# Performance work log

Measured on AMD Instinct MI355X. Metric: run time of the kernel, lower is better.

Reference implementation:

```python
import jax, jax.numpy as jnp
import numpy as np

DIM = 256
HEADS = 8
DHEAD = 64
MEM = 4
HID = HEADS * DHEAD  # 512


def setup_inputs() -> dict:
    key = jax.random.key(0)
    k1, k2, k3, k4 = jax.random.split(key, 4)
    x = jax.random.normal(k1, (2, DIM, 48, 48), jnp.float32)
    gamma = jnp.zeros((DIM, 1, 1), jnp.float32)  # nn.Parameter init is zeros
    mem_kv = jax.random.normal(k2, (2, HEADS, MEM, DHEAD), jnp.float32)
    w_qkv = jax.random.normal(k3, (3 * HID, DIM), jnp.float32) * 0.05  # 1x1 conv weight
    w_out = jax.random.normal(k4, (DIM, HID), jnp.float32) * 0.05     # 1x1 conv weight
    return {"x": x, "gamma": gamma, "mem_kv": mem_kv, "w_qkv": w_qkv, "w_out": w_out}


def reference(x, gamma, mem_kv, w_qkv, w_out):
    b, c, h, w = x.shape
    scale = DHEAD ** -0.5
    # RMSNorm: F.normalize along channel dim (L2, eps=1e-12) * (gamma+1) * sqrt(dim)
    l2 = jnp.sqrt(jnp.sum(x * x, axis=1, keepdims=True))
    xn = x / jnp.maximum(l2, 1e-12) * (gamma + 1.0) * (c ** 0.5)
    # 1x1 conv to qkv: [b, 3*HID, h, w]
    qkv = jnp.einsum('oc,bchw->bohw', w_qkv, xn)
    qkv = qkv.reshape(b, 3, HEADS, DHEAD, h * w)
    # (b, heads, n, dhead)
    q = jnp.swapaxes(qkv[:, 0], 2, 3)
    k = jnp.swapaxes(qkv[:, 1], 2, 3)
    v = jnp.swapaxes(qkv[:, 2], 2, 3)
    # prepend learnable memory kv tokens
    mk = jnp.broadcast_to(mem_kv[0], (b, HEADS, MEM, DHEAD))
    mv = jnp.broadcast_to(mem_kv[1], (b, HEADS, MEM, DHEAD))
    k = jnp.concatenate([mk, k], axis=2)
    v = jnp.concatenate([mv, v], axis=2)
    sim = jnp.einsum('bhid,bhjd->bhij', q * scale, k)
    attn = jax.nn.softmax(sim, axis=-1)
    out = jnp.einsum('bhij,bhjd->bhid', attn, v)
    out = jnp.swapaxes(out, 2, 3).reshape(b, HID, h, w)
    return jnp.einsum('oc,bchw->bohw', w_out, out)
```

## Files before the change

### kernel.cpp

```cpp
#include <hip/hip_runtime.h>

#define BATCH 2
#define CDIM 256
#define NPIX 2304
#define NHEAD 8
#define DH 64
#define HID 512
#define NMEM 4
#define NKV 2308
#define NKVP 2368
#define QSCALE 0.125f
#define LOG2E 1.4426950408889634f
#define WQKV_E 393216
#define WOUT_E 131072
#define KVSPLIT 1216

typedef float f32x4 __attribute__((ext_vector_type(4)));
typedef __bf16 bf16x8 __attribute__((ext_vector_type(8)));
typedef unsigned short u16;
typedef u16 u16x4 __attribute__((ext_vector_type(4)));
typedef u16 u16x8 __attribute__((ext_vector_type(8)));
typedef unsigned u32x2 __attribute__((ext_vector_type(2)));

#if __has_builtin(__builtin_amdgcn_exp2f)
#define EXP2(x) __builtin_amdgcn_exp2f(x)
#else
#define EXP2(x) exp2f(x)
#endif

static __device__ __forceinline__ u16 f2b(float f) {
  union { float f; unsigned u; } a; a.f = f;
  unsigned u = a.u;
  u += 0x7fffu + ((u >> 16) & 1u);
  return (u16)(u >> 16);
}

__global__ __launch_bounds__(256) void k_prep(
    const float* __restrict__ wqkv, const float* __restrict__ wout,
    const float* __restrict__ gamma, const float* __restrict__ mem_kv,
    u16* __restrict__ wb, u16* __restrict__ kk, u16* __restrict__ vT)
{
  const int blk = blockIdx.x, t = threadIdx.x;
  if (blk < 256) {
    const int i0 = (blk * 256 + t) * 8;
    u16x8 o;
    if (i0 < WQKV_E) {
      const float sc = ((i0 >> 8) < 512) ? QSCALE * LOG2E : 1.0f;
      const int c0 = i0 & 255;
      const f32x4 a = *(const f32x4*)&wqkv[i0];
      const f32x4 b = *(const f32x4*)&wqkv[i0 + 4];
      const f32x4 g0 = *(const f32x4*)&gamma[c0];
      const f32x4 g1 = *(const f32x4*)&gamma[c0 + 4];
#pragma unroll
      for (int e = 0; e < 4; ++e) {
        o[e]     = f2b(a[e] * sc * (1.0f + g0[e]));
        o[e + 4] = f2b(b[e] * sc * (1.0f + g1[e]));
      }
    } else {
      const f32x4 a = *(const f32x4*)&wout[i0 - WQKV_E];
      const f32x4 b = *(const f32x4*)&wout[i0 - WQKV_E + 4];
#pragma unroll
      for (int e = 0; e < 4; ++e) { o[e] = f2b(a[e]); o[e + 4] = f2b(b[e]); }
    }
    *(u16x8*)&wb[i0] = o;
  } else if (blk < 272) {
    const int idx = (blk - 256) * 256 + t;
    const int d = idx & 63;
    const int m = (idx >> 6) & 3;
    const int h = (idx >> 8) & 7;
    const int b = idx >> 11;
    const float mk = mem_kv[((size_t)h * NMEM + m) * DH + d];
    const float mv = mem_kv[(((size_t)NHEAD + h) * NMEM + m) * DH + d];
    kk[(((size_t)(b * NHEAD + h)) * NKV + m) * DH + d] = f2b(mk);
    vT[(((size_t)(b * NHEAD + h)) * DH + d) * NKVP + m] = f2b(mv);
  } else {
    const int gid = (blk - 272) * 256 + t;
    const int row = gid >> 4;
    const int c0 = (gid & 15) * 4 + 2304;
    u16x4 z = {0, 0, 0, 0};
    *(u16x4*)&vT[(size_t)row * NKVP + c0] = z;
  }
}

__global__ __launch_bounds__(256) void k_norm(
    const float* __restrict__ x, u16* __restrict__ xnT)
{
  __shared__ float xs[16 * 261];
  __shared__ float red[16][17];
  __shared__ float rsh[16];
  const int t = threadIdx.x;
  const int blk = blockIdx.x;
  const int b = blk / 144;
  const int p0 = (blk % 144) * 16;
  const int px = t & 15, cg = t >> 4;
  const float* xb = x + (size_t)b * CDIM * NPIX + p0 + px;
  float ssq = 0.f;
#pragma unroll
  for (int i = 0; i < 16; ++i) {
    const int c = cg * 16 + i;
    const float v = xb[(size_t)c * NPIX];
    xs[px * 261 + c] = v;
    ssq += v * v;
  }
  red[px][cg] = ssq;
  __syncthreads();
  if (t < 16) {
    float s = 0.f;
#pragma unroll
    for (int i = 0; i < 16; ++i) s += red[t][i];
    rsh[t] = 16.0f / fmaxf(sqrtf(s), 1e-12f);
  }
  __syncthreads();
  {
    const int pp = t >> 4, c0 = (t & 15) * 16;
    const float rs = rsh[pp];
    u16x8 o0, o1;
#pragma unroll
    for (int e = 0; e < 8; ++e) {
      o0[e] = f2b(xs[pp * 261 + c0 + e] * rs);
      o1[e] = f2b(xs[pp * 261 + c0 + 8 + e] * rs);
    }
    u16* dst = &xnT[(size_t)(b * NPIX + p0 + pp) * CDIM + c0];
    *(u16x8*)dst = o0;
    *(u16x8*)(dst + 8) = o1;
  }
}

__global__ __launch_bounds__(256) void k_qkv(
    const u16* __restrict__ xnT, const u16* __restrict__ wb,
    u16* __restrict__ q, u16* __restrict__ kk, u16* __restrict__ vT)
{
  __shared__ __align__(16) u16 bs[64 * 256];
  const int t = threadIdx.x, w = t >> 6, l = t & 63, li = l & 15, kg = l >> 4;
  const int m0 = blockIdx.x * 64 + w * 16;
  const int n0 = blockIdx.y * 64;
  {
    const int brow = t >> 2, bcs = (t & 3) * 64;
    const int bsw = (brow & 7) * 8;
    const u16* wsrc = wb + (size_t)(n0 + brow) * CDIM + bcs;
#pragma unroll
    for (int j = 0; j < 8; ++j) {
      const u16x8 v = *(const u16x8*)&wsrc[j * 8];
      *(u16x8*)&bs[brow * 256 + ((bcs + j * 8) ^ bsw)] = v;
    }
  }
  const u16* ap = xnT + (size_t)(m0 + li) * CDIM + kg * 8;
  const int lsw = (li & 7) * 8;
  f32x4 acc[4];
#pragma unroll
  for (int cf = 0; cf < 4; ++cf) { f32x4 z = {0.f,0.f,0.f,0.f}; acc[cf] = z; }
  __syncthreads();
#pragma unroll
  for (int ks = 0; ks < 8; ++ks) {
    const bf16x8 af = *(const bf16x8*)(ap + ks * 32);
#pragma unroll
    for (int cf = 0; cf < 4; ++cf) {
      const int row = cf * 16 + li;
      const bf16x8 bfr = *(const bf16x8*)&bs[row * 256 + ((ks * 32 + kg * 8) ^ lsw)];
      acc[cf] = __builtin_amdgcn_mfma_f32_16x16x32_bf16(af, bfr, acc[cf], 0, 0, 0);
    }
  }
  const int bb = (m0 >= NPIX) ? 1 : 0;
  const int plbase = m0 - bb * NPIX + kg * 4;
#pragma unroll
  for (int cf = 0; cf < 4; ++cf) {
    const int o0f = n0 + cf * 16;
    const int r = o0f >> 9, oo = o0f & 511, h = oo >> 6, d = (oo & 63) + li;
    if (r == 0) {
      u16* base = q + ((size_t)(bb * NHEAD + h) * NPIX + plbase) * DH + d;
#pragma unroll
      for (int rr = 0; rr < 4; ++rr) base[(size_t)rr * DH] = f2b(acc[cf][rr]);
    } else if (r == 1) {
      u16* base = kk + ((size_t)(bb * NHEAD + h) * NKV + NMEM + plbase) * DH + d;
#pragma unroll
      for (int rr = 0; rr < 4; ++rr) base[(size_t)rr * DH] = f2b(acc[cf][rr]);
    } else {
      u16x4 pk;
#pragma unroll
      for (int rr = 0; rr < 4; ++rr) pk[rr] = f2b(acc[cf][rr]);
      *(u16x4*)&vT[(((size_t)(bb * NHEAD + h)) * DH + d) * NKVP + NMEM + plbase] = pk;
    }
  }
}

__global__ __launch_bounds__(512) void k_attn(
    const u16* __restrict__ q, const u16* __restrict__ kk, const u16* __restrict__ vT,
    u16* __restrict__ aoB)
{
  __shared__ __align__(16) char smem[51200];
  u16* kbuf = (u16*)smem;
  u16* vbuf = (u16*)(smem + 16384);
  u16* ps   = (u16*)(smem + 32768);
  float* accbuf = (float*)smem;
  float* mlbuf  = (float*)(smem + 17152);
  const int t = threadIdx.x;
  const int w = t >> 6, l = t & 63;
  const int qsub = w & 3, hf = w >> 2;
  const int li = l & 15, kg = l >> 4;
  const int id = blockIdx.x;
  const int xcd = id & 7, slot = id >> 3;
  const int yl = (slot >= 36) ? 1 : 0;
  const int xq = slot - yl * 36;
  const int bh = xcd * 2 + yl;
  const int b = bh >> 3, hh = bh & 7;
  const int qrow0 = xq * 64 + qsub * 16;
  const u16* qp = q + ((size_t)bh * NPIX + qrow0) * DH;
  const u16* kp = kk + (size_t)bh * NKV * DH;
  const u16* vp = vT + (size_t)bh * DH * NKVP;

  const bf16x8 bq0 = *(const bf16x8*)&qp[li * DH + kg * 8];
  const bf16x8 bq1 = *(const bf16x8*)&qp[li * DH + 32 + kg * 8];

  const int hft = t >> 8;
  const int tt = t & 255;
  const int srow = tt >> 3;
  const int scol = (tt & 7) * 8;
  const int ssw = (srow & 7) * 8;
  const int sbase = hft * KVSPLIT;
  u16* kdst0 = &kbuf[hft * 4096 + srow * 64 + (scol ^ ssw)];
  u16* kdst1 = &kbuf[hft * 4096 + (srow + 32) * 64 + (scol ^ ssw)];
  u16* vdst0 = &vbuf[hft * 4096 + srow * 64 + (scol ^ ssw)];
  u16* vdst1 = &vbuf[hft * 4096 + (srow + 32) * 64 + (scol ^ ssw)];

  f32x4 acc[4];
#pragma unroll
  for (int df = 0; df < 4; ++df) { f32x4 z = {0.f,0.f,0.f,0.f}; acc[df] = z; }
  float m = -1e30f, lsum = 0.f;
  const int cbase0 = hf * KVSPLIT;

  u16x8 rk0, rk1, rv0, rv1;
  rk0 = *(const u16x8*)&kp[(size_t)(sbase + srow) * DH + scol];
  rk1 = *(const u16x8*)&kp[(size_t)(sbase + srow + 32) * DH + scol];
  rv0 = *(const u16x8*)&vp[(size_t)srow * NKVP + sbase + scol];
  rv1 = *(const u16x8*)&vp[(size_t)(srow + 32) * NKVP + sbase + scol];

  const int NT = 19;
  for (int i = 0; i < NT; ++i) {
    __syncthreads();
    *(u16x8*)kdst0 = rk0;
    *(u16x8*)kdst1 = rk1;
    *(u16x8*)vdst0 = rv0;
    *(u16x8*)vdst1 = rv1;
    if (i + 1 < NT) {
      int nb = sbase + (i + 1) * 64;
      int snb = (nb > NKVP - 64) ? (NKVP - 64) : nb;
      int kr0 = nb + srow;      if (kr0 > NKV - 1) kr0 = NKV - 1;
      int kr1 = nb + srow + 32; if (kr1 > NKV - 1) kr1 = NKV - 1;
      rk0 = *(const u16x8*)&kp[(size_t)kr0 * DH + scol];
      rk1 = *(const u16x8*)&kp[(size_t)kr1 * DH + scol];
      rv0 = *(const u16x8*)&vp[(size_t)srow * NKVP + snb + scol];
      rv1 = *(const u16x8*)&vp[(size_t)(srow + 32) * NKVP + snb + scol];
    }
    __syncthreads();
    const int kbase = cbase0 + i * 64;
    if (kbase < NKV) {
      const bool lastt = (kbase + 64 > NKV);
      const u16* kb = &kbuf[hf * 4096];
      const u16* vb = &vbuf[hf * 4096];
      f32x4 s[4];
#pragma unroll
      for (int jf = 0; jf < 4; ++jf) {
        const int row = jf * 16 + li;
        const int rsw = (row & 7) * 8;
        const bf16x8 ak0 = *(const bf16x8*)&kb[row * 64 + ((kg * 8) ^ rsw)];
        const bf16x8 ak1 = *(const bf16x8*)&kb[row * 64 + ((32 + kg * 8) ^ rsw)];
        f32x4 sf = {0.f, 0.f, 0.f, 0.f};
        sf = __builtin_amdgcn_mfma_f32_16x16x32_bf16(ak0, bq0, sf, 0, 0, 0);
        sf = __builtin_amdgcn_mfma_f32_16x16x32_bf16(ak1, bq1, sf, 0, 0, 0);
        s[jf] = sf;
      }
      if (lastt) {
#pragma unroll
        for (int jf = 0; jf < 4; ++jf)
#pragma unroll
          for (int r = 0; r < 4; ++r)
            if (kbase + jf * 16 + kg * 4 + r >= NKV) s[jf][r] = -1e30f;
      }
      float pmax = fmaxf(fmaxf(fmaxf(s[0][0], s[0][1]), fmaxf(s[0][2], s[0][3])),
                         fmaxf(fmaxf(s[1][0], s[1][1]), fmaxf(s[1][2], s[1][3])));
      pmax = fmaxf(pmax, fmaxf(fmaxf(fmaxf(s[2][0], s[2][1]), fmaxf(s[2][2], s[2][3])),
                               fmaxf(fmaxf(s[3][0], s[3][1]), fmaxf(s[3][2], s[3][3]))));
      pmax = fmaxf(pmax, __shfl_xor(pmax, 16));
      pmax = fmaxf(pmax, __shfl_xor(pmax, 32));
      if (__any(pmax > m + 8.0f)) {
        const float mn = fmaxf(m, pmax);
        const float al = EXP2(m - mn);
        m = mn;
        lsum *= al;
        float a4[4];
#pragma unroll
        for (int r = 0; r < 4; ++r) a4[r] = __shfl(al, (l & 48) | (kg * 4 + r));
#pragma unroll
        for (int df = 0; df < 4; ++df)
#pragma unroll
          for (int r = 0; r < 4; ++r) acc[df][r] *= a4[r];
      }
#pragma unroll
      for (int jf = 0; jf < 4; ++jf) {
        u32x2 wp;
#pragma unroll
        for (int rp = 0; rp < 2; ++rp) {
          const float e0 = EXP2(s[jf][rp * 2 + 0] - m);
          const float e1 = EXP2(s[jf][rp * 2 + 1] - m);
          lsum += e0 + e1;
          unsigned pk;
          asm("v_cvt_pk_bf16_f32 %0, %1, %2" : "=v"(pk) : "v"(e0), "v"(e1));
          wp[rp] = pk;
        }
        *(u32x2*)&ps[w * 1152 + li * 72 + jf * 16 + kg * 4] = wp;
      }
      asm volatile("s_waitcnt lgkmcnt(0)" ::: "memory");
      __builtin_amdgcn_sched_barrier(0);
      const bf16x8 ap0 = *(const bf16x8*)&ps[w * 1152 + li * 72 + kg * 8];
      const bf16x8 ap1 = *(const bf16x8*)&ps[w * 1152 + li * 72 + 32 + kg * 8];
#pragma unroll
      for (int df = 0; df < 4; ++df) {
        const int row = df * 16 + li;
        const int rsw = (row & 7) * 8;
        const bf16x8 bv0 = *(const bf16x8*)&vb[row * 64 + ((kg * 8) ^ rsw)];
        const bf16x8 bv1 = *(const bf16x8*)&vb[row * 64 + ((32 + kg * 8) ^ rsw)];
        acc[df] = __builtin_amdgcn_mfma_f32_16x16x32_bf16(ap0, bv0, acc[df], 0, 0, 0);
        acc[df] = __builtin_amdgcn_mfma_f32_16x16x32_bf16(ap1, bv1, acc[df], 0, 0, 0);
      }
    }
  }
  lsum += __shfl_xor(lsum, 16);
  lsum += __shfl_xor(lsum, 32);
  float m4[4], l4[4];
#pragma unroll
  for (int r = 0; r < 4; ++r) {
    const int src = (l & 48) | (kg * 4 + r);
    m4[r] = __shfl(m, src);
    l4[r] = __shfl(lsum, src);
  }
  __syncthreads();
  if (hf == 1) {
#pragma unroll
    for (int df = 0; df < 4; ++df)
#pragma unroll
      for (int r = 0; r < 4; ++r)
        accbuf[(qsub * 16 + kg * 4 + r) * 67 + df * 16 + li] = acc[df][r];
    if (kg == 0) {
      mlbuf[(qsub * 16 + li) * 2 + 0] = m;
      mlbuf[(qsub * 16 + li) * 2 + 1] = lsum;
    }
  }
  __syncthreads();
  if (hf == 0) {
    float f0[4], f1[4], rL[4];
#pragma unroll
    for (int r = 0; r < 4; ++r) {
      const float m1 = mlbuf[(qsub * 16 + kg * 4 + r) * 2 + 0];
      const float l1 = mlbuf[(qsub * 16 + kg * 4 + r) * 2 + 1];
      const float M = fmaxf(m4[r], m1);
      f0[r] = EXP2(m4[r] - M);
      f1[r] = EXP2(m1 - M);
      rL[r] = __builtin_amdgcn_rcpf(l4[r] * f0[r] + l1 * f1[r]);
    }
#pragma unroll
    for (int df = 0; df < 4; ++df)
#pragma unroll
      for (int r = 0; r < 4; ++r) {
        const float a1 = accbuf[(qsub * 16 + kg * 4 + r) * 67 + df * 16 + li];
        const float o = (acc[df][r] * f0[r] + a1 * f1[r]) * rL[r];
        aoB[((size_t)b * NPIX + qrow0 + kg * 4 + r) * HID + hh * DH + df * 16 + li] = f2b(o);
      }
  }
}

__global__ __launch_bounds__(256) void k_outg(
    const u16* __restrict__ aoB, const u16* __restrict__ wob, float* __restrict__ out)
{
  const int t = threadIdx.x, w = t >> 6, l = t & 63, li = l & 15, kg = l >> 4;
  const int wm = w >> 1, wn = w & 1;
  const int m0 = blockIdx.x * 32 + wm * 16;
  const int n0 = blockIdx.y * 32 + wn * 16;
  const u16* ap = aoB + (size_t)(m0 + li) * HID + kg * 8;
  const u16* bp = wob + (size_t)(n0 + li) * HID + kg * 8;
  f32x4 acc = {0.f, 0.f, 0.f, 0.f};
#pragma unroll
  for (int ks = 0; ks < 16; ++ks) {
    const bf16x8 af = *(const bf16x8*)(ap + ks * 32);
    const bf16x8 bf = *(const bf16x8*)(bp + ks * 32);
    acc = __builtin_amdgcn_mfma_f32_16x16x32_bf16(af, bf, acc, 0, 0, 0);
  }
  const int bb = (m0 >= NPIX) ? 1 : 0;
  const int pl = m0 - bb * NPIX + kg * 4;
  const int o = n0 + li;
  *(f32x4*)&out[((size_t)(bb * CDIM + o)) * NPIX + pl] = acc;
}

extern "C" void kernel_launch(void* const* d_in, const int* in_sizes, int n_in,
                              void* d_out, int out_size, void* d_ws, size_t ws_size,
                              hipStream_t stream)
{
  const float* x      = (const float*)d_in[0];
  const float* gamma  = (const float*)d_in[1];
  const float* mem_kv = (const float*)d_in[2];
  const float* wqkv   = (const float*)d_in[3];
  const float* wout   = (const float*)d_in[4];
  float* out = (float*)d_out;
  char* ws = (char*)d_ws;
  const size_t XNT = (size_t)BATCH * NPIX * CDIM * sizeof(u16);
  const size_t WB  = (size_t)(WQKV_E + WOUT_E) * sizeof(u16);
  const size_t QB  = (size_t)BATCH * NHEAD * NPIX * DH * sizeof(u16);
  const size_t KB  = (size_t)BATCH * NHEAD * NKV  * DH * sizeof(u16);
  const size_t VTB = (size_t)BATCH * NHEAD * DH * NKVP * sizeof(u16);
  u16* xnT = (u16*)ws;
  u16* wb  = (u16*)(ws + XNT);
  u16* q   = (u16*)(ws + XNT + WB);
  u16* kk  = (u16*)(ws + XNT + WB + QB);
  u16* vT  = (u16*)(ws + XNT + WB + QB + KB);
  u16* aoB = (u16*)(ws + XNT + WB + QB + KB + VTB);

  k_prep<<<dim3(336), dim3(256), 0, stream>>>(wqkv, wout, gamma, mem_kv, wb, kk, vT);
  k_norm<<<dim3(288), dim3(256), 0, stream>>>(x, xnT);
  k_qkv<<<dim3(72, 24), dim3(256), 0, stream>>>(xnT, wb, q, kk, vT);
  k_attn<<<dim3(576), dim3(512), 0, stream>>>(q, kk, vT, aoB);
  k_outg<<<dim3(144, 8), dim3(256), 0, stream>>>(aoB, wb + WQKV_E, out);
}
```

Before: 104.4 us.

## Switch attention kernel to 32x32x16 MFMA with register-resident P

Rewrites the attention inner loop to use 32x32x16 bf16 MFMA tiles, giving each wave 32 query rows instead of 16 and halving the block to 256 threads. The softmax probabilities now stay in registers, with a lane-xor-32 shuffle rearranging them into the B operand layout, so the LDS round trip through the ps buffer and its waitcnt/sched barrier are gone. The row max and sum reductions become mostly in-register, and the final merge uses vectorized LDS and global stores. The cost is more accumulator registers per wave (two f32x16 accumulators plus two f32x16 score tiles), which may lower occupancy, and fewer waves per block to hide load latency.

```diff
diff --git a/kernel.cpp b/kernel.cpp
--- a/kernel.cpp
+++ b/kernel.cpp
@@ -16,11 +16,12 @@
 #define KVSPLIT 1216
 
 typedef float f32x4 __attribute__((ext_vector_type(4)));
+typedef float f32x16 __attribute__((ext_vector_type(16)));
 typedef __bf16 bf16x8 __attribute__((ext_vector_type(8)));
 typedef unsigned short u16;
 typedef u16 u16x4 __attribute__((ext_vector_type(4)));
 typedef u16 u16x8 __attribute__((ext_vector_type(8)));
-typedef unsigned u32x2 __attribute__((ext_vector_type(2)));
+typedef unsigned u32x4 __attribute__((ext_vector_type(4)));
 
 #if __has_builtin(__builtin_amdgcn_exp2f)
 #define EXP2(x) __builtin_amdgcn_exp2f(x)
@@ -183,73 +184,76 @@
   }
 }
 
-__global__ __launch_bounds__(512) void k_attn(
+__global__ __launch_bounds__(256) void k_attn(
     const u16* __restrict__ q, const u16* __restrict__ kk, const u16* __restrict__ vT,
     u16* __restrict__ aoB)
 {
-  __shared__ __align__(16) char smem[51200];
+  __shared__ __align__(16) char smem[32768];
   u16* kbuf = (u16*)smem;
   u16* vbuf = (u16*)(smem + 16384);
-  u16* ps   = (u16*)(smem + 32768);
   float* accbuf = (float*)smem;
-  float* mlbuf  = (float*)(smem + 17152);
+  float* mlbuf  = (float*)(smem + 16640);
   const int t = threadIdx.x;
   const int w = t >> 6, l = t & 63;
-  const int qsub = w & 3, hf = w >> 2;
-  const int li = l & 15, kg = l >> 4;
+  const int qsub = w & 1, hf = w >> 1;
+  const int lq = l & 31, hi = l >> 5;
   const int id = blockIdx.x;
   const int xcd = id & 7, slot = id >> 3;
   const int yl = (slot >= 36) ? 1 : 0;
   const int xq = slot - yl * 36;
   const int bh = xcd * 2 + yl;
   const int b = bh >> 3, hh = bh & 7;
-  const int qrow0 = xq * 64 + qsub * 16;
-  const u16* qp = q + ((size_t)bh * NPIX + qrow0) * DH;
+  const int qrow0 = xq * 64 + qsub * 32;
+  const u16* qp = q + ((size_t)bh * NPIX + qrow0 + lq) * DH;
   const u16* kp = kk + (size_t)bh * NKV * DH;
   const u16* vp = vT + (size_t)bh * DH * NKVP;
 
-  const bf16x8 bq0 = *(const bf16x8*)&qp[li * DH + kg * 8];
-  const bf16x8 bq1 = *(const bf16x8*)&qp[li * DH + 32 + kg * 8];
-
-  const int hft = t >> 8;
-  const int tt = t & 255;
-  const int srow = tt >> 3;
-  const int scol = (tt & 7) * 8;
+  bf16x8 bq[4];
+#pragma unroll
+  for (int ks = 0; ks < 4; ++ks) bq[ks] = *(const bf16x8*)&qp[ks * 16 + hi * 8];
+
+  const int hft = t >> 7;
+  const int tt = t & 127;
+  const int srow = tt >> 1;
+  const int c0 = (tt & 1) * 4;
   const int ssw = (srow & 7) * 8;
   const int sbase = hft * KVSPLIT;
-  u16* kdst0 = &kbuf[hft * 4096 + srow * 64 + (scol ^ ssw)];
-  u16* kdst1 = &kbuf[hft * 4096 + (srow + 32) * 64 + (scol ^ ssw)];
-  u16* vdst0 = &vbuf[hft * 4096 + srow * 64 + (scol ^ ssw)];
-  u16* vdst1 = &vbuf[hft * 4096 + (srow + 32) * 64 + (scol ^ ssw)];
-
-  f32x4 acc[4];
-#pragma unroll
-  for (int df = 0; df < 4; ++df) { f32x4 z = {0.f,0.f,0.f,0.f}; acc[df] = z; }
+  u16* kdst = &kbuf[hft * 4096 + srow * 64];
+  u16* vdst = &vbuf[hft * 4096 + srow * 64];
+
+  f32x16 acc0, acc1;
+#pragma unroll
+  for (int r = 0; r < 16; ++r) { acc0[r] = 0.f; acc1[r] = 0.f; }
   float m = -1e30f, lsum = 0.f;
   const int cbase0 = hf * KVSPLIT;
 
-  u16x8 rk0, rk1, rv0, rv1;
-  rk0 = *(const u16x8*)&kp[(size_t)(sbase + srow) * DH + scol];
-  rk1 = *(const u16x8*)&kp[(size_t)(sbase + srow + 32) * DH + scol];
-  rv0 = *(const u16x8*)&vp[(size_t)srow * NKVP + sbase + scol];
-  rv1 = *(const u16x8*)&vp[(size_t)(srow + 32) * NKVP + sbase + scol];
+  u16x8 pk[4], pv[4];
+#pragma unroll
+  for (int j = 0; j < 4; ++j) {
+    const int cc = (c0 + j) * 8;
+    pk[j] = *(const u16x8*)&kp[(size_t)(sbase + srow) * DH + cc];
+    pv[j] = *(const u16x8*)&vp[(size_t)srow * NKVP + sbase + cc];
+  }
 
   const int NT = 19;
   for (int i = 0; i < NT; ++i) {
     __syncthreads();
-    *(u16x8*)kdst0 = rk0;
-    *(u16x8*)kdst1 = rk1;
-    *(u16x8*)vdst0 = rv0;
-    *(u16x8*)vdst1 = rv1;
+#pragma unroll
+    for (int j = 0; j < 4; ++j) {
+      const int cc = (c0 + j) * 8;
+      *(u16x8*)&kdst[cc ^ ssw] = pk[j];
+      *(u16x8*)&vdst[cc ^ ssw] = pv[j];
+    }
     if (i + 1 < NT) {
-      int nb = sbase + (i + 1) * 64;
-      int snb = (nb > NKVP - 64) ? (NKVP - 64) : nb;
-      int kr0 = nb + srow;      if (kr0 > NKV - 1) kr0 = NKV - 1;
-      int kr1 = nb + srow + 32; if (kr1 > NKV - 1) kr1 = NKV - 1;
-      rk0 = *(const u16x8*)&kp[(size_t)kr0 * DH + scol];
-      rk1 = *(const u16x8*)&kp[(size_t)kr1 * DH + scol];
-      rv0 = *(const u16x8*)&vp[(size_t)srow * NKVP + snb + scol];
-      rv1 = *(const u16x8*)&vp[(size_t)(srow + 32) * NKVP + snb + scol];
+      const int nb = sbase + (i + 1) * 64;
+      const int snb = (nb > NKVP - 64) ? (NKVP - 64) : nb;
+      int kr = nb + srow; if (kr > NKV - 1) kr = NKV - 1;
+#pragma unroll
+      for (int j = 0; j < 4; ++j) {
+        const int cc = (c0 + j) * 8;
+        pk[j] = *(const u16x8*)&kp[(size_t)kr * DH + cc];
+        pv[j] = *(const u16x8*)&vp[(size_t)srow * NKVP + snb + cc];
+      }
     }
     __syncthreads();
     const int kbase = cbase0 + i * 64;
@@ -257,114 +261,130 @@
       const bool lastt = (kbase + 64 > NKV);
       const u16* kb = &kbuf[hf * 4096];
       const u16* vb = &vbuf[hf * 4096];
-      f32x4 s[4];
-#pragma unroll
-      for (int jf = 0; jf < 4; ++jf) {
-        const int row = jf * 16 + li;
-        const int rsw = (row & 7) * 8;
-        const bf16x8 ak0 = *(const bf16x8*)&kb[row * 64 + ((kg * 8) ^ rsw)];
-        const bf16x8 ak1 = *(const bf16x8*)&kb[row * 64 + ((32 + kg * 8) ^ rsw)];
-        f32x4 sf = {0.f, 0.f, 0.f, 0.f};
-        sf = __builtin_amdgcn_mfma_f32_16x16x32_bf16(ak0, bq0, sf, 0, 0, 0);
-        sf = __builtin_amdgcn_mfma_f32_16x16x32_bf16(ak1, bq1, sf, 0, 0, 0);
-        s[jf] = sf;
+      const int lsw = (lq & 7) * 8;
+      f32x16 s0, s1;
+#pragma unroll
+      for (int r = 0; r < 16; ++r) { s0[r] = 0.f; s1[r] = 0.f; }
+#pragma unroll
+      for (int ks = 0; ks < 4; ++ks) {
+        const int col = (ks * 16 + hi * 8) ^ lsw;
+        const bf16x8 ak0 = *(const bf16x8*)&kb[lq * 64 + col];
+        const bf16x8 ak1 = *(const bf16x8*)&kb[(32 + lq) * 64 + col];
+        s0 = __builtin_amdgcn_mfma_f32_32x32x16_bf16(ak0, bq[ks], s0, 0, 0, 0);
+        s1 = __builtin_amdgcn_mfma_f32_32x32x16_bf16(ak1, bq[ks], s1, 0, 0, 0);
       }
       if (lastt) {
 #pragma unroll
-        for (int jf = 0; jf < 4; ++jf)
-#pragma unroll
-          for (int r = 0; r < 4; ++r)
-            if (kbase + jf * 16 + kg * 4 + r >= NKV) s[jf][r] = -1e30f;
-      }
-      float pmax = fmaxf(fmaxf(fmaxf(s[0][0], s[0][1]), fmaxf(s[0][2], s[0][3])),
-                         fmaxf(fmaxf(s[1][0], s[1][1]), fmaxf(s[1][2], s[1][3])));
-      pmax = fmaxf(pmax, fmaxf(fmaxf(fmaxf(s[2][0], s[2][1]), fmaxf(s[2][2], s[2][3])),
-                               fmaxf(fmaxf(s[3][0], s[3][1]), fmaxf(s[3][2], s[3][3]))));
-      pmax = fmaxf(pmax, __shfl_xor(pmax, 16));
+        for (int g = 0; g < 4; ++g)
+#pragma unroll
+          for (int rr = 0; rr < 4; ++rr) {
+            const int row = rr + 8 * g + 4 * hi;
+            if (kbase + row >= NKV) s0[g * 4 + rr] = -1e30f;
+            if (kbase + 32 + row >= NKV) s1[g * 4 + rr] = -1e30f;
+          }
+      }
+      float v[16];
+#pragma unroll
+      for (int r = 0; r < 16; ++r) v[r] = fmaxf(s0[r], s1[r]);
+#pragma unroll
+      for (int st = 8; st > 0; st >>= 1)
+#pragma unroll
+        for (int r = 0; r < 8; ++r) if (r < st) v[r] = fmaxf(v[r], v[r + st]);
+      float pmax = v[0];
       pmax = fmaxf(pmax, __shfl_xor(pmax, 32));
       if (__any(pmax > m + 8.0f)) {
         const float mn = fmaxf(m, pmax);
         const float al = EXP2(m - mn);
         m = mn;
         lsum *= al;
-        float a4[4];
-#pragma unroll
-        for (int r = 0; r < 4; ++r) a4[r] = __shfl(al, (l & 48) | (kg * 4 + r));
-#pragma unroll
-        for (int df = 0; df < 4; ++df)
-#pragma unroll
-          for (int r = 0; r < 4; ++r) acc[df][r] *= a4[r];
-      }
-#pragma unroll
-      for (int jf = 0; jf < 4; ++jf) {
-        u32x2 wp;
-#pragma unroll
-        for (int rp = 0; rp < 2; ++rp) {
-          const float e0 = EXP2(s[jf][rp * 2 + 0] - m);
-          const float e1 = EXP2(s[jf][rp * 2 + 1] - m);
-          lsum += e0 + e1;
-          unsigned pk;
-          asm("v_cvt_pk_bf16_f32 %0, %1, %2" : "=v"(pk) : "v"(e0), "v"(e1));
-          wp[rp] = pk;
-        }
-        *(u32x2*)&ps[w * 1152 + li * 72 + jf * 16 + kg * 4] = wp;
-      }
-      asm volatile("s_waitcnt lgkmcnt(0)" ::: "memory");
-      __builtin_amdgcn_sched_barrier(0);
-      const bf16x8 ap0 = *(const bf16x8*)&ps[w * 1152 + li * 72 + kg * 8];
-      const bf16x8 ap1 = *(const bf16x8*)&ps[w * 1152 + li * 72 + 32 + kg * 8];
-#pragma unroll
-      for (int df = 0; df < 4; ++df) {
-        const int row = df * 16 + li;
-        const int rsw = (row & 7) * 8;
-        const bf16x8 bv0 = *(const bf16x8*)&vb[row * 64 + ((kg * 8) ^ rsw)];
-        const bf16x8 bv1 = *(const bf16x8*)&vb[row * 64 + ((32 + kg * 8) ^ rsw)];
-        acc[df] = __builtin_amdgcn_mfma_f32_16x16x32_bf16(ap0, bv0, acc[df], 0, 0, 0);
-        acc[df] = __builtin_amdgcn_mfma_f32_16x16x32_bf16(ap1, bv1, acc[df], 0, 0, 0);
-      }
-    }
-  }
-  lsum += __shfl_xor(lsum, 16);
+#pragma unroll
+        for (int r = 0; r < 16; ++r) { acc0[r] *= al; acc1[r] *= al; }
+      }
+      unsigned q0[8], q1[8];
+      float ps8[8];
+#pragma unroll
+      for (int r2 = 0; r2 < 8; ++r2) {
+        const float a0 = EXP2(s0[2 * r2] - m), a1 = EXP2(s0[2 * r2 + 1] - m);
+        const float b0 = EXP2(s1[2 * r2] - m), b1 = EXP2(s1[2 * r2 + 1] - m);
+        unsigned u0, u1;
+        asm("v_cvt_pk_bf16_f32 %0, %1, %2" : "=v"(u0) : "v"(a0), "v"(a1));
+        asm("v_cvt_pk_bf16_f32 %0, %1, %2" : "=v"(u1) : "v"(b0), "v"(b1));
+        q0[r2] = u0; q1[r2] = u1;
+        ps8[r2] = (a0 + a1) + (b0 + b1);
+      }
+      lsum += ((ps8[0] + ps8[1]) + (ps8[2] + ps8[3])) +
+              ((ps8[4] + ps8[5]) + (ps8[6] + ps8[7]));
+      unsigned rx0[2][2], rx1[2][2];
+#pragma unroll
+      for (int j = 0; j < 2; ++j) {
+        const unsigned s00 = hi ? q0[4 * j]     : q0[4 * j + 2];
+        const unsigned s01 = hi ? q0[4 * j + 1] : q0[4 * j + 3];
+        const unsigned s10 = hi ? q1[4 * j]     : q1[4 * j + 2];
+        const unsigned s11 = hi ? q1[4 * j + 1] : q1[4 * j + 3];
+        rx0[j][0] = __shfl_xor(s00, 32);
+        rx0[j][1] = __shfl_xor(s01, 32);
+        rx1[j][0] = __shfl_xor(s10, 32);
+        rx1[j][1] = __shfl_xor(s11, 32);
+      }
+      bf16x8 bp[4];
+#pragma unroll
+      for (int sub = 0; sub < 2; ++sub) {
+        u32x4 wv;
+        wv[0] = hi ? rx0[sub][0] : q0[4 * sub];
+        wv[1] = hi ? rx0[sub][1] : q0[4 * sub + 1];
+        wv[2] = hi ? q0[4 * sub + 2] : rx0[sub][0];
+        wv[3] = hi ? q0[4 * sub + 3] : rx0[sub][1];
+        bp[sub] = *(bf16x8*)&wv;
+        u32x4 wv1;
+        wv1[0] = hi ? rx1[sub][0] : q1[4 * sub];
+        wv1[1] = hi ? rx1[sub][1] : q1[4 * sub + 1];
+        wv1[2] = hi ? q1[4 * sub + 2] : rx1[sub][0];
+        wv1[3] = hi ? q1[4 * sub + 3] : rx1[sub][1];
+        bp[2 + sub] = *(bf16x8*)&wv1;
+      }
+#pragma unroll
+      for (int ks = 0; ks < 4; ++ks) {
+        const int col = (ks * 16 + hi * 8) ^ lsw;
+        const bf16x8 av0 = *(const bf16x8*)&vb[lq * 64 + col];
+        const bf16x8 av1 = *(const bf16x8*)&vb[(32 + lq) * 64 + col];
+        acc0 = __builtin_amdgcn_mfma_f32_32x32x16_bf16(av0, bp[ks], acc0, 0, 0, 0);
+        acc1 = __builtin_amdgcn_mfma_f32_32x32x16_bf16(av1, bp[ks], acc1, 0, 0, 0);
+      }
+    }
+  }
   lsum += __shfl_xor(lsum, 32);
-  float m4[4], l4[4];
-#pragma unroll
-  for (int r = 0; r < 4; ++r) {
-    const int src = (l & 48) | (kg * 4 + r);
-    m4[r] = __shfl(m, src);
-    l4[r] = __shfl(lsum, src);
-  }
+  const int ql = qsub * 32 + lq;
   __syncthreads();
   if (hf == 1) {
 #pragma unroll
-    for (int df = 0; df < 4; ++df)
-#pragma unroll
-      for (int r = 0; r < 4; ++r)
-        accbuf[(qsub * 16 + kg * 4 + r) * 67 + df * 16 + li] = acc[df][r];
-    if (kg == 0) {
-      mlbuf[(qsub * 16 + li) * 2 + 0] = m;
-      mlbuf[(qsub * 16 + li) * 2 + 1] = lsum;
-    }
+    for (int g = 0; g < 4; ++g) {
+      f32x4 qa = {acc0[4 * g], acc0[4 * g + 1], acc0[4 * g + 2], acc0[4 * g + 3]};
+      f32x4 qb = {acc1[4 * g], acc1[4 * g + 1], acc1[4 * g + 2], acc1[4 * g + 3]};
+      *(f32x4*)&accbuf[ql * 65 + 8 * g + 4 * hi] = qa;
+      *(f32x4*)&accbuf[ql * 65 + 32 + 8 * g + 4 * hi] = qb;
+    }
+    if (!hi) { mlbuf[ql * 2] = m; mlbuf[ql * 2 + 1] = lsum; }
   }
   __syncthreads();
   if (hf == 0) {
-    float f0[4], f1[4], rL[4];
-#pragma unroll
-    for (int r = 0; r < 4; ++r) {
-      const float m1 = mlbuf[(qsub * 16 + kg * 4 + r) * 2 + 0];
-      const float l1 = mlbuf[(qsub * 16 + kg * 4 + r) * 2 + 1];
-      const float M = fmaxf(m4[r], m1);
-      f0[r] = EXP2(m4[r] - M);
-      f1[r] = EXP2(m1 - M);
-      rL[r] = __builtin_amdgcn_rcpf(l4[r] * f0[r] + l1 * f1[r]);
-    }
-#pragma unroll
-    for (int df = 0; df < 4; ++df)
-#pragma unroll
-      for (int r = 0; r < 4; ++r) {
-        const float a1 = accbuf[(qsub * 16 + kg * 4 + r) * 67 + df * 16 + li];
-        const float o = (acc[df][r] * f0[r] + a1 * f1[r]) * rL[r];
-        aoB[((size_t)b * NPIX + qrow0 + kg * 4 + r) * HID + hh * DH + df * 16 + li] = f2b(o);
-      }
+    const float m1 = mlbuf[ql * 2], l1 = mlbuf[ql * 2 + 1];
+    const float M = fmaxf(m, m1);
+    const float f0 = EXP2(m - M), f1 = EXP2(m1 - M);
+    const float rL = __builtin_amdgcn_rcpf(lsum * f0 + l1 * f1);
+    u16* obase = aoB + ((size_t)b * NPIX + qrow0 + lq) * HID + hh * DH;
+#pragma unroll
+    for (int g = 0; g < 4; ++g) {
+      const f32x4 a1a = *(const f32x4*)&accbuf[ql * 65 + 8 * g + 4 * hi];
+      const f32x4 a1b = *(const f32x4*)&accbuf[ql * 65 + 32 + 8 * g + 4 * hi];
+      u16x4 oa, ob;
+#pragma unroll
+      for (int rr = 0; rr < 4; ++rr) {
+        oa[rr] = f2b((acc0[4 * g + rr] * f0 + a1a[rr] * f1) * rL);
+        ob[rr] = f2b((acc1[4 * g + rr] * f0 + a1b[rr] * f1) * rL);
+      }
+      *(u16x4*)&obase[8 * g + 4 * hi] = oa;
+      *(u16x4*)&obase[32 + 8 * g + 4 * hi] = ob;
+    }
   }
 }
 
@@ -416,6 +436,6 @@
   k_prep<<<dim3(336), dim3(256), 0, stream>>>(wqkv, wout, gamma, mem_kv, wb, kk, vT);
   k_norm<<<dim3(288), dim3(256), 0, stream>>>(x, xnT);
   k_qkv<<<dim3(72, 24), dim3(256), 0, stream>>>(xnT, wb, q, kk, vT);
-  k_attn<<<dim3(576), dim3(512), 0, stream>>>(q, kk, vT, aoB);
+  k_attn<<<dim3(576), dim3(256), 0, stream>>>(q, kk, vT, aoB);
   k_outg<<<dim3(144, 8), dim3(256), 0, stream>>>(aoB, wb + WQKV_E, out);
 }
```

Measured after the change: 121.1 us. +16.0%, slower.
